# Kernel optimization log

Hardware: AMD Instinct MI355X
Metric: run time of the kernel (lower is better)

Reference implementation:

```python
import jax, jax.numpy as jnp
import numpy as np

SIGMA = 3.0
NUM_CLASSES = 10


def _nearest_resize(x, out_h, out_w):
    # torch F.interpolate default 'nearest': src_idx = floor(dst_idx * in/out)
    in_h, in_w = x.shape[-2], x.shape[-1]
    rows = (jnp.arange(out_h) * in_h) // out_h
    cols = (jnp.arange(out_w) * in_w) // out_w
    return x[..., rows, :][..., :, cols]


def _forward(feats, centers, idx, labels, img_h, img_w):
    # Gaussian heatmap per user input at image resolution: [B,N,H,W]
    xs = jnp.arange(img_w, dtype=jnp.float32) + 0.5  # pixel-centre xs
    ys = jnp.arange(img_h, dtype=jnp.float32) + 0.5
    alpha = -0.5 / (SIGMA ** 2)
    cx = centers[..., 0][..., None, None]  # [B,N,1,1]
    cy = centers[..., 1][..., None, None]
    heat = jnp.exp(alpha * ((xs[None, None, None, :] - cx) ** 2
                            + (ys[None, None, :, None] - cy) ** 2))
    valid = (idx != -1)[..., None, None]  # idx == -1 rows stay zero
    heat = jnp.where(valid, heat, jnp.zeros((), heat.dtype))

    cls_ids = jnp.arange(1, NUM_CLASSES + 1)
    cmask = labels[:, None, :] == cls_ids[None, :, None]  # [B,K,N]
    any_cls = jnp.any(cmask, axis=-1)                     # [B,K]

    outs = []
    for feat in feats:
        H, W = feat.shape[-2], feat.shape[-1]
        h = _nearest_resize(heat, H, W)                               # [B,N,H,W]
        h = h / (jnp.sum(h, axis=(-2, -1), keepdims=True) + 1e-8)
        # template (eq 1): spatially weighted average feature vector
        tmpl = jnp.einsum('bchw,bnhw->bnc', feat, h)                  # [B,N,C]
        # correlation (eq 2): 1x1 conv of feat with per-sample template
        cor = jnp.einsum('bnc,bchw->bnhw', tmpl, feat)                # [B,N,H,W]
        # class-wise collate: max over user inputs whose label == class
        neg = jnp.finfo(cor.dtype).min
        masked = jnp.where(cmask[..., None, None], cor[:, None], neg)  # [B,K,N,H,W]
        cmax = jnp.max(masked, axis=2)                                 # [B,K,H,W]
        cmax = jnp.where(any_cls[..., None, None], cmax, jnp.zeros((), cmax.dtype))
        outs.append(jnp.concatenate([feat, cmax], axis=1))             # [B,C+K,H,W]
    return tuple(outs)


def setup_inputs() -> dict:
    key = jax.random.key(0)
    k0, k1, k2, kc, ki, kl = jax.random.split(key, 6)
    B, C, N = 2, 256, 64
    img_h, img_w = 512, 512
    x0 = jax.random.normal(k0, (B, C, 64, 64), dtype=jnp.float32)
    x1 = jax.random.normal(k1, (B, C, 32, 32), dtype=jnp.float32)
    x2 = jax.random.normal(k2, (B, C, 16, 16), dtype=jnp.float32)
    centers = jax.random.uniform(kc, (B, N, 2), dtype=jnp.float32) * jnp.array([img_w, img_h], dtype=jnp.float32)
    idx = jnp.where(jax.random.uniform(ki, (B, N)) < 0.1, -1, 0).astype(jnp.int64)
    labels = jax.random.randint(kl, (B, N), 1, NUM_CLASSES + 1).astype(jnp.int64)
    return {"x0": x0, "x1": x1, "x2": x2, "centers": centers,
            "idx": idx, "labels": labels, "img_h": img_h, "img_w": img_w}


def reference(x0, x1, x2, centers, idx, labels, img_h, img_w):
    return _forward((x0, x1, x2), centers, idx, labels, img_h, img_w)
```

## Files before the change

### kernel.cpp

```cpp
#include <hip/hip_runtime.h>
#include <hip/hip_bf16.h>
#include <cfloat>
#include <cmath>

namespace {
constexpr int NB = 2;
constexpr int NN = 64;
constexpr int NC = 256;
constexpr int NK = 10;
constexpr float ALPHA = -1.0f / 18.0f;
constexpr int TMPL_FLOATS = 3 * NB * NC * NN;
}

__device__ __forceinline__ bool sniff_f32(const void* x0) {
  const ushort4 v = ((const ushort4*)x0)[threadIdx.x & 63];
  bool bad = (((v.x >> 7) & 0xFF) >= 137) | (((v.y >> 7) & 0xFF) >= 137) |
             (((v.z >> 7) & 0xFF) >= 137) | (((v.w >> 7) & 0xFF) >= 137);
  return __ballot(bad) != 0ULL;
}

__device__ __forceinline__ float ldf(const void* p, size_t i, bool f32) {
  return f32 ? ((const float*)p)[i]
             : __bfloat162float(((const __hip_bfloat16*)p)[i]);
}

__global__ __launch_bounds__(256) void tmpl_kernel(
    const void* __restrict__ x0, const void* __restrict__ x1,
    const void* __restrict__ x2, const void* __restrict__ centers,
    const int* __restrict__ idxp, const int* __restrict__ labels,
    float* __restrict__ tmpl_t) {
  const bool f32 = sniff_f32(x0);
  const int bx  = blockIdx.x;
  const int lvl = bx >> 7;
  const int b   = (bx >> 6) & 1;
  const int n   = bx & 63;
  const int W   = 64 >> lvl;
  const int HW  = W * W;
  const float s = (float)(8 << lvl);
  const void* feat = (lvl == 0) ? x0 : (lvl == 1) ? x1 : x2;

  __shared__ float ex[64], ey[64];
  __shared__ float sh_inv;
  __shared__ int   sh_win[4];

  const int t = threadIdx.x;
  const float cx = ldf(centers, (size_t)(b * NN + n) * 2 + 0, f32);
  const float cy = ldf(centers, (size_t)(b * NN + n) * 2 + 1, f32);

  if (t < W) {
    const float dx = (float)t * s + 0.5f - cx;
    const float dy = (float)t * s + 0.5f - cy;
    ex[t] = expf(ALPHA * dx * dx);
    ey[t] = expf(ALPHA * dy * dy);
  }
  __syncthreads();

  if (t == 0) {
    const bool i64 = (labels[1] == 0);
    const int  m   = b * NN + n;
    const int  iv  = i64 ? idxp[2 * m] : idxp[m];
    float Sx = 0.f, Sy = 0.f;
    for (int i = 0; i < W; ++i) { Sx += ex[i]; Sy += ey[i]; }
    sh_inv = (iv != -1) ? 1.0f / (Sx * Sy + 1e-8f) : 0.0f;
    int cs = (int)floorf((cx - 0.5f) / s + 0.5f); cs = min(max(cs, 0), W - 1);
    int rs = (int)floorf((cy - 0.5f) / s + 0.5f); rs = min(max(rs, 0), W - 1);
    const float tx = ex[cs] * 1e-7f, ty = ey[rs] * 1e-7f;
    int clo = cs, chi = cs, rlo = rs, rhi = rs;
    while (clo > 0     && ex[clo - 1] >= tx) --clo;
    while (chi < W - 1 && ex[chi + 1] >= tx) ++chi;
    while (rlo > 0     && ey[rlo - 1] >= ty) --rlo;
    while (rhi < W - 1 && ey[rhi + 1] >= ty) ++rhi;
    sh_win[0] = clo; sh_win[1] = chi; sh_win[2] = rlo; sh_win[3] = rhi;
  }
  __syncthreads();

  const float inv = sh_inv;
  const int clo = sh_win[0], chi = sh_win[1], rlo = sh_win[2], rhi = sh_win[3];
  const size_t cbase = (size_t)(b * NC + t) * HW;
  float acc = 0.f;
  for (int r = rlo; r <= rhi; ++r) {
    float rowa = 0.f;
    for (int c = clo; c <= chi; ++c)
      rowa += ex[c] * ldf(feat, cbase + r * W + c, f32);
    acc += ey[r] * rowa;
  }
  tmpl_t[(((size_t)lvl * NB + b) * NC + t) * NN + n] = acc * inv;
}

__global__ __launch_bounds__(1024, 1) void cor_kernel(
    const void* __restrict__ x0, const void* __restrict__ x1,
    const void* __restrict__ x2, const int* __restrict__ labels,
    const float* __restrict__ tmpl_t, float* __restrict__ out) {
  const bool f32 = sniff_f32(x0);
  const int bx = blockIdx.x;
  int lvl, b, tile;
  if (bx < 128)      { lvl = 0; b = bx >> 6;  tile = bx & 63; }
  else if (bx < 160) { const int l = bx - 128; lvl = 1; b = l >> 4; tile = l & 15; }
  else               { const int l = bx - 160; lvl = 2; b = l >> 2; tile = l & 3; }
  const int W = 64 >> lvl, HW = W * W;
  const int lane = threadIdx.x & 63;
  const int wv  = __builtin_amdgcn_readfirstlane(threadIdx.x >> 6);
  const int nch = wv & 3;
  const int cq  = wv >> 2;
  const int p = tile * 64 + lane;
  const void* feat = (lvl == 0) ? x0 : (lvl == 1) ? x1 : x2;
  const size_t base1 = (size_t)NB * (NC + NK) * 4096;
  const size_t base2 = base1 + (size_t)NB * (NC + NK) * 1024;
  const size_t lvl_base = (lvl == 0) ? 0 : (lvl == 1) ? base1 : base2;
  float* ob = out + lvl_base + (size_t)b * (NC + NK) * HW + p;
  const size_t fb = (size_t)b * NC * HW + p;
  const float* tw = tmpl_t + (size_t)(lvl * NB + b) * NC * NN + 16 * nch;

  __shared__ float part[4][NN][64];
  __shared__ float kmb[4][NK][64];
  __shared__ int   lab[NN];
  if (threadIdx.x < NN) {
    const bool i64 = (labels[1] == 0);
    const int  m   = b * NN + threadIdx.x;
    lab[threadIdx.x] = i64 ? labels[2 * m] : labels[m];
  }

  float acc[16];
#pragma unroll
  for (int i = 0; i < 16; ++i) acc[i] = 0.f;

  auto kloop = [&](auto* pf) {
#pragma unroll 8
    for (int i = 0; i < 64; ++i) {
      const int c = cq * 64 + i;
      const float f = (float)pf[fb + (size_t)c * HW];
      if (nch == 0) ob[(size_t)c * HW] = f;
      const float4* t4p = (const float4*)(tw + c * NN);
#pragma unroll
      for (int j = 0; j < 4; ++j) {
        const float4 t4 = t4p[j];
        acc[4 * j + 0] += t4.x * f;
        acc[4 * j + 1] += t4.y * f;
        acc[4 * j + 2] += t4.z * f;
        acc[4 * j + 3] += t4.w * f;
      }
    }
  };
  if (f32) kloop((const float*)feat);
  else     kloop((const __hip_bfloat16*)feat);

#pragma unroll
  for (int i = 0; i < 16; ++i) part[cq][16 * nch + i][lane] = acc[i];
  __syncthreads();

  if (cq == 0) {
    float km[NK];
#pragma unroll
    for (int k = 0; k < NK; ++k) km[k] = -FLT_MAX;
#pragma unroll
    for (int i = 0; i < 16; ++i) {
      const int n = 16 * nch + i;
      const float tot = part[0][n][lane] + part[1][n][lane]
                      + part[2][n][lane] + part[3][n][lane];
      const int L = lab[n];
#pragma unroll
      for (int kk = 1; kk <= NK; ++kk)
        if (L == kk) km[kk - 1] = fmaxf(km[kk - 1], tot);
    }
#pragma unroll
    for (int k = 0; k < NK; ++k) kmb[nch][k][lane] = km[k];
  }
  __syncthreads();

  if (wv == 0) {
#pragma unroll
    for (int k = 0; k < NK; ++k) {
      const float m = fmaxf(fmaxf(kmb[0][k][lane], kmb[1][k][lane]),
                            fmaxf(kmb[2][k][lane], kmb[3][k][lane]));
      ob[(size_t)(NC + k) * HW] = (m == -FLT_MAX) ? 0.f : m;
    }
  }
}

extern "C" void kernel_launch(void* const* d_in, const int* in_sizes, int n_in,
                              void* d_out, int out_size, void* d_ws, size_t ws_size,
                              hipStream_t stream) {
  const void* x0 = d_in[0];
  const void* x1 = d_in[1];
  const void* x2 = d_in[2];
  const void* ce = d_in[3];
  const int* idxp   = (const int*)d_in[4];
  const int* labels = (const int*)d_in[5];
  float* tmpl = (float*)d_ws;
  float* out  = (float*)d_out;

  tmpl_kernel<<<3 * NB * NN, 256, 0, stream>>>(x0, x1, x2, ce, idxp, labels, tmpl);
  cor_kernel<<<168, 1024, 0, stream>>>(x0, x1, x2, labels, tmpl, out);
}
```

Before: 109.3 us.

## Stage per-batch templates in LDS and software-prefetch feature loads in correlation kernel

```diff
diff --git a/kernel.cpp b/kernel.cpp
--- a/kernel.cpp
+++ b/kernel.cpp
@@ -109,36 +109,53 @@
   const size_t lvl_base = (lvl == 0) ? 0 : (lvl == 1) ? base1 : base2;
   float* ob = out + lvl_base + (size_t)b * (NC + NK) * HW + p;
   const size_t fb = (size_t)b * NC * HW + p;
-  const float* tw = tmpl_t + (size_t)(lvl * NB + b) * NC * NN + 16 * nch;
-
+
+  __shared__ float tlds[NC][NN];
   __shared__ float part[4][NN][64];
   __shared__ float kmb[4][NK][64];
   __shared__ int   lab[NN];
+
+  {
+    const float4* src4 =
+        (const float4*)(tmpl_t + (size_t)(lvl * NB + b) * NC * NN);
+    float4* dst4 = (float4*)&tlds[0][0];
+#pragma unroll
+    for (int k = 0; k < 4; ++k)
+      dst4[threadIdx.x + k * 1024] = src4[threadIdx.x + k * 1024];
+  }
   if (threadIdx.x < NN) {
     const bool i64 = (labels[1] == 0);
     const int  m   = b * NN + threadIdx.x;
     lab[threadIdx.x] = i64 ? labels[2 * m] : labels[m];
   }
+  __syncthreads();
 
   float acc[16];
 #pragma unroll
   for (int i = 0; i < 16; ++i) acc[i] = 0.f;
 
   auto kloop = [&](auto* pf) {
-#pragma unroll 8
+    float fpre[4];
+#pragma unroll
+    for (int k = 0; k < 4; ++k)
+      fpre[k] = (float)pf[fb + (size_t)(cq * 64 + k) * HW];
+#pragma unroll 4
     for (int i = 0; i < 64; ++i) {
       const int c = cq * 64 + i;
-      const float f = (float)pf[fb + (size_t)c * HW];
+      const float f = fpre[i & 3];
+      const int cnx = min(c + 4, NC - 1);
+      fpre[i & 3] = (float)pf[fb + (size_t)cnx * HW];
       if (nch == 0) ob[(size_t)c * HW] = f;
-      const float4* t4p = (const float4*)(tw + c * NN);
-#pragma unroll
-      for (int j = 0; j < 4; ++j) {
-        const float4 t4 = t4p[j];
-        acc[4 * j + 0] += t4.x * f;
-        acc[4 * j + 1] += t4.y * f;
-        acc[4 * j + 2] += t4.z * f;
-        acc[4 * j + 3] += t4.w * f;
-      }
+      const float4* t4p = (const float4*)&tlds[c][16 * nch];
+      const float4 t0 = t4p[0], t1 = t4p[1], t2 = t4p[2], t3 = t4p[3];
+      acc[0]  += t0.x * f; acc[1]  += t0.y * f;
+      acc[2]  += t0.z * f; acc[3]  += t0.w * f;
+      acc[4]  += t1.x * f; acc[5]  += t1.y * f;
+      acc[6]  += t1.z * f; acc[7]  += t1.w * f;
+      acc[8]  += t2.x * f; acc[9]  += t2.y * f;
+      acc[10] += t2.z * f; acc[11] += t2.w * f;
+      acc[12] += t3.x * f; acc[13] += t3.y * f;
+      acc[14] += t3.z * f; acc[15] += t3.w * f;
     }
   };
   if (f32) kloop((const float*)feat);
```

After: 100.3 us. 1.09x faster.

## Split correlation into per-channel-quarter partial kernel plus separate combine kernel

Applied to the files above, without the earlier changes.

```diff
diff --git a/kernel.cpp b/kernel.cpp
--- a/kernel.cpp
+++ b/kernel.cpp
@@ -10,6 +10,9 @@
 constexpr int NK = 10;
 constexpr float ALPHA = -1.0f / 18.0f;
 constexpr int TMPL_FLOATS = 3 * NB * NC * NN;
+constexpr int PQ  = NB * NN * (4096 + 1024 + 256);
+constexpr int PL1 = NB * NN * 4096;
+constexpr int PL2 = PL1 + NB * NN * 1024;
 }
 
 __device__ __forceinline__ bool sniff_f32(const void* x0) {
@@ -22,6 +25,9 @@
 __device__ __forceinline__ float ldf(const void* p, size_t i, bool f32) {
   return f32 ? ((const float*)p)[i]
              : __bfloat162float(((const __hip_bfloat16*)p)[i]);
+}
+__device__ __forceinline__ float bf2f(unsigned short u) {
+  return __uint_as_float((unsigned)u << 16);
 }
 
 __global__ __launch_bounds__(256) void tmpl_kernel(
@@ -87,87 +93,131 @@
   tmpl_t[(((size_t)lvl * NB + b) * NC + t) * NN + n] = acc * inv;
 }
 
-__global__ __launch_bounds__(1024, 1) void cor_kernel(
+__global__ __launch_bounds__(256, 1) void cor_part_kernel(
     const void* __restrict__ x0, const void* __restrict__ x1,
-    const void* __restrict__ x2, const int* __restrict__ labels,
-    const float* __restrict__ tmpl_t, float* __restrict__ out) {
+    const void* __restrict__ x2, const float* __restrict__ tmpl_t,
+    float* __restrict__ part, float* __restrict__ out) {
   const bool f32 = sniff_f32(x0);
-  const int bx = blockIdx.x;
-  int lvl, b, tile;
-  if (bx < 128)      { lvl = 0; b = bx >> 6;  tile = bx & 63; }
-  else if (bx < 160) { const int l = bx - 128; lvl = 1; b = l >> 4; tile = l & 15; }
-  else               { const int l = bx - 160; lvl = 2; b = l >> 2; tile = l & 3; }
+  const int bx   = blockIdx.x;
+  const int tile = bx >> 2, q = bx & 3;
+  int lvl, b, tl;
+  if (tile < 32)      { lvl = 0; b = tile >> 4; tl = tile & 15; }
+  else if (tile < 40) { const int l = tile - 32; lvl = 1; b = l >> 2; tl = l & 3; }
+  else                { lvl = 2; b = tile - 40; tl = 0; }
   const int W = 64 >> lvl, HW = W * W;
   const int lane = threadIdx.x & 63;
-  const int wv  = __builtin_amdgcn_readfirstlane(threadIdx.x >> 6);
-  const int nch = wv & 3;
-  const int cq  = wv >> 2;
-  const int p = tile * 64 + lane;
+  const int nch  = __builtin_amdgcn_readfirstlane(threadIdx.x >> 6);
+  const int px   = tl * 256 + lane * 4;
   const void* feat = (lvl == 0) ? x0 : (lvl == 1) ? x1 : x2;
   const size_t base1 = (size_t)NB * (NC + NK) * 4096;
   const size_t base2 = base1 + (size_t)NB * (NC + NK) * 1024;
   const size_t lvl_base = (lvl == 0) ? 0 : (lvl == 1) ? base1 : base2;
-  float* ob = out + lvl_base + (size_t)b * (NC + NK) * HW + p;
-  const size_t fb = (size_t)b * NC * HW + p;
-  const float* tw = tmpl_t + (size_t)(lvl * NB + b) * NC * NN + 16 * nch;
-
-  __shared__ float part[4][NN][64];
+  float* ob = out + lvl_base + (size_t)b * (NC + NK) * HW + px;
+  const int c0 = q * 64;
+  const size_t pbase = (lvl == 0) ? 0 : (lvl == 1) ? PL1 : PL2;
+  float* pp = part + (size_t)q * PQ + pbase + (size_t)b * NN * HW + px;
+
+  __shared__ float tlds[64][64];
+  {
+    const float4* s4 =
+        (const float4*)(tmpl_t + ((size_t)(lvl * NB + b) * NC + c0) * NN);
+    float4* d4 = (float4*)&tlds[0][0];
+#pragma unroll
+    for (int k = 0; k < 4; ++k)
+      d4[threadIdx.x + k * 256] = s4[threadIdx.x + k * 256];
+  }
+  __syncthreads();
+
+  float4 acc[16];
+#pragma unroll
+  for (int j = 0; j < 16; ++j) acc[j] = float4{0.f, 0.f, 0.f, 0.f};
+
+  auto run = [&](auto loadf) {
+    float4 fpre[2];
+    fpre[0] = loadf(c0);
+    fpre[1] = loadf(c0 + 1);
+#pragma unroll 4
+    for (int i = 0; i < 64; ++i) {
+      const int c = c0 + i;
+      const float4 f = fpre[i & 1];
+      fpre[i & 1] = loadf(min(c + 2, NC - 1));
+      if (nch == 0) *(float4*)&ob[(size_t)c * HW] = f;
+#pragma unroll
+      for (int j = 0; j < 16; ++j) {
+        const float tv = tlds[i][16 * nch + j];
+        acc[j].x += tv * f.x; acc[j].y += tv * f.y;
+        acc[j].z += tv * f.z; acc[j].w += tv * f.w;
+      }
+    }
+  };
+  if (f32) {
+    const float4* fp4 =
+        (const float4*)((const float*)feat + (size_t)b * NC * HW + px);
+    const int st = HW >> 2;
+    run([&](int c) { return fp4[(size_t)c * st]; });
+  } else {
+    const ushort4* hp4 =
+        (const ushort4*)((const unsigned short*)feat + (size_t)b * NC * HW + px);
+    const int st = HW >> 2;
+    run([&](int c) {
+      const ushort4 v = hp4[(size_t)c * st];
+      return float4{bf2f(v.x), bf2f(v.y), bf2f(v.z), bf2f(v.w)};
+    });
+  }
+
+#pragma unroll
+  for (int j = 0; j < 16; ++j)
+    *(float4*)&pp[(size_t)(16 * nch + j) * HW] = acc[j];
+}
+
+__global__ __launch_bounds__(256) void combine_kernel(
+    const int* __restrict__ labels, const float* __restrict__ part,
+    float* __restrict__ out) {
+  const int bx   = blockIdx.x;
+  const int tile = bx >> 2, pq = bx & 3;
+  int lvl, b, tl;
+  if (tile < 32)      { lvl = 0; b = tile >> 4; tl = tile & 15; }
+  else if (tile < 40) { const int l = tile - 32; lvl = 1; b = l >> 2; tl = l & 3; }
+  else                { lvl = 2; b = tile - 40; tl = 0; }
+  const int W = 64 >> lvl, HW = W * W;
+  const int lane = threadIdx.x & 63;
+  const int nch  = __builtin_amdgcn_readfirstlane(threadIdx.x >> 6);
+  const int px   = tl * 256 + pq * 64 + lane;
+  const size_t base1 = (size_t)NB * (NC + NK) * 4096;
+  const size_t base2 = base1 + (size_t)NB * (NC + NK) * 1024;
+  const size_t lvl_base = (lvl == 0) ? 0 : (lvl == 1) ? base1 : base2;
+  float* ob = out + lvl_base + (size_t)b * (NC + NK) * HW + px;
+  const size_t pbase = (lvl == 0) ? 0 : (lvl == 1) ? PL1 : PL2;
+  const float* pp = part + pbase + (size_t)b * NN * HW + px;
+
+  __shared__ int   lab[NN];
   __shared__ float kmb[4][NK][64];
-  __shared__ int   lab[NN];
   if (threadIdx.x < NN) {
     const bool i64 = (labels[1] == 0);
     const int  m   = b * NN + threadIdx.x;
     lab[threadIdx.x] = i64 ? labels[2 * m] : labels[m];
   }
-
-  float acc[16];
-#pragma unroll
-  for (int i = 0; i < 16; ++i) acc[i] = 0.f;
-
-  auto kloop = [&](auto* pf) {
-#pragma unroll 8
-    for (int i = 0; i < 64; ++i) {
-      const int c = cq * 64 + i;
-      const float f = (float)pf[fb + (size_t)c * HW];
-      if (nch == 0) ob[(size_t)c * HW] = f;
-      const float4* t4p = (const float4*)(tw + c * NN);
-#pragma unroll
-      for (int j = 0; j < 4; ++j) {
-        const float4 t4 = t4p[j];
-        acc[4 * j + 0] += t4.x * f;
-        acc[4 * j + 1] += t4.y * f;
-        acc[4 * j + 2] += t4.z * f;
-        acc[4 * j + 3] += t4.w * f;
-      }
-    }
-  };
-  if (f32) kloop((const float*)feat);
-  else     kloop((const __hip_bfloat16*)feat);
-
-#pragma unroll
-  for (int i = 0; i < 16; ++i) part[cq][16 * nch + i][lane] = acc[i];
-  __syncthreads();
-
-  if (cq == 0) {
-    float km[NK];
-#pragma unroll
-    for (int k = 0; k < NK; ++k) km[k] = -FLT_MAX;
-#pragma unroll
-    for (int i = 0; i < 16; ++i) {
-      const int n = 16 * nch + i;
-      const float tot = part[0][n][lane] + part[1][n][lane]
-                      + part[2][n][lane] + part[3][n][lane];
-      const int L = lab[n];
-#pragma unroll
-      for (int kk = 1; kk <= NK; ++kk)
-        if (L == kk) km[kk - 1] = fmaxf(km[kk - 1], tot);
-    }
-#pragma unroll
-    for (int k = 0; k < NK; ++k) kmb[nch][k][lane] = km[k];
-  }
-  __syncthreads();
-
-  if (wv == 0) {
+  __syncthreads();
+
+  float km[NK];
+#pragma unroll
+  for (int k = 0; k < NK; ++k) km[k] = -FLT_MAX;
+#pragma unroll 4
+  for (int i = 0; i < 16; ++i) {
+    const int n = 16 * nch + i;
+    const size_t o = (size_t)n * HW;
+    const float tot = pp[o] + pp[(size_t)PQ + o] + pp[2 * (size_t)PQ + o]
+                    + pp[3 * (size_t)PQ + o];
+    const int L = lab[n];
+#pragma unroll
+    for (int kk = 1; kk <= NK; ++kk)
+      if (L == kk) km[kk - 1] = fmaxf(km[kk - 1], tot);
+  }
+#pragma unroll
+  for (int k = 0; k < NK; ++k) kmb[nch][k][lane] = km[k];
+  __syncthreads();
+
+  if (nch == 0) {
 #pragma unroll
     for (int k = 0; k < NK; ++k) {
       const float m = fmaxf(fmaxf(kmb[0][k][lane], kmb[1][k][lane]),
@@ -187,8 +237,10 @@
   const int* idxp   = (const int*)d_in[4];
   const int* labels = (const int*)d_in[5];
   float* tmpl = (float*)d_ws;
+  float* part = tmpl + TMPL_FLOATS;
   float* out  = (float*)d_out;
 
   tmpl_kernel<<<3 * NB * NN, 256, 0, stream>>>(x0, x1, x2, ce, idxp, labels, tmpl);
-  cor_kernel<<<168, 1024, 0, stream>>>(x0, x1, x2, labels, tmpl, out);
-}
+  cor_part_kernel<<<168, 256, 0, stream>>>(x0, x1, x2, tmpl, part, out);
+  combine_kernel<<<168, 256, 0, stream>>>(labels, part, out);
+}
```

Result: no change. 108.2 us (-1.0%).
